# Kernel optimization log

Hardware: AMD Instinct MI355X
Metric: run time of the kernel (lower is better)

The kernel has to match this reference:

```python
import jax, jax.numpy as jnp
import numpy as np

B, T, C, H = 16, 2048, 1024, 64  # batch, seq (== block_size), n_embd, head_size


def setup_inputs() -> dict:
    key = jax.random.key(0)
    ks = jax.random.split(key, 4)
    s = 1.0 / np.sqrt(C)  # Linear default init scale
    return {
        "x": jax.random.normal(ks[0], (B, T, C), dtype=jnp.float32),
        "Wq": jax.random.normal(ks[1], (C, H), dtype=jnp.float32) * s,
        "bq": jnp.zeros((H,), dtype=jnp.float32),
        "Wk": jax.random.normal(ks[2], (C, H), dtype=jnp.float32) * s,
        "bk": jnp.zeros((H,), dtype=jnp.float32),
        "Wv": jax.random.normal(ks[3], (C, H), dtype=jnp.float32) * s,
        "bv": jnp.zeros((H,), dtype=jnp.float32),
    }


def reference(x, Wq, bq, Wk, bk, Wv, bv):
    # q, k, v: (B, T, H)
    q = x @ Wq + bq
    k = x @ Wk + bk
    v = x @ Wv + bv
    # scores (B, T, T); NOTE: original code has NO 1/sqrt(H) scaling
    wei = jnp.einsum("btd,bsd->bts", q, k)
    t = x.shape[1]
    causal = jnp.tril(jnp.ones((t, t), dtype=bool))
    wei = jnp.where(causal, wei, -jnp.inf)
    # NOTE: original code applies softmax over dim=1 (query axis), kept faithfully
    wei = jax.nn.softmax(wei, axis=1)
    # dropout is identity at p=0 / eval
    out = jnp.einsum("bts,bsd->btd", wei, v)  # (B, T, H)
    return out
```

## Files before the change

### kernel.cpp

```cpp
#include <hip/hip_runtime.h>
#include <hip/hip_bf16.h>
#include <math.h>

#define TT 2048
#define NB 16

typedef short short8 __attribute__((ext_vector_type(8)));
typedef float f32x4 __attribute__((ext_vector_type(4)));
typedef unsigned short us4 __attribute__((ext_vector_type(4)));

#define MFMA16(a,b,c) __builtin_amdgcn_mfma_f32_16x16x32_bf16((a),(b),(c),0,0,0)

typedef const __attribute__((address_space(1))) unsigned gas_u32;
typedef __attribute__((address_space(3))) unsigned las_u32;

__device__ __forceinline__ void gll16(const void* g, void* l) {
    __builtin_amdgcn_global_load_lds((gas_u32*)g, (las_u32*)l, 16, 0, 0);
}

__device__ __forceinline__ unsigned short bf16rn(float f) {
    unsigned u = __float_as_uint(f);
    u += 0x7FFFu + ((u >> 16) & 1u);
    return (unsigned short)(u >> 16);
}
__device__ __forceinline__ float bf16tof(unsigned short h) {
    return __uint_as_float(((unsigned)h) << 16);
}

__device__ __forceinline__ int strip_base(int i) {
    int h = i >> 1;
    return h * (h + 1) + (i & 1) * (h + 1);
}

__global__ void wprep_kernel(const float* __restrict__ Wq,
                             const float* __restrict__ Wk,
                             const float* __restrict__ Wv,
                             short* __restrict__ WT)
{
    const int m = blockIdx.x >> 6, n = blockIdx.x & 63, tid = threadIdx.x;
    const float* W = (m == 0) ? Wq : ((m == 1) ? Wk : Wv);
    const float sc = (m == 0) ? 1.4426950408889634f : 1.f;
    const int k0 = tid * 4;
    us4 hv, lv;
#pragma unroll
    for (int r = 0; r < 4; ++r) {
        float v = W[(size_t)(k0 + r) * 64 + n] * sc;
        unsigned short hh = bf16rn(v);
        hv[r] = hh;
        lv[r] = bf16rn(v - bf16tof(hh));
    }
    *(us4*)&WT[((size_t)(m * 2 + 0) * 64 + n) * 1024 + k0] = hv;
    *(us4*)&WT[((size_t)(m * 2 + 1) * 64 + n) * 1024 + k0] = lv;
}

__global__ void zero_kernel(float* __restrict__ p) {
    p[blockIdx.x * 256 + threadIdx.x] = 0.f;
}

__global__ __launch_bounds__(256, 2) void qkv_kernel(
    const float* __restrict__ x,
    const float* __restrict__ bq, const float* __restrict__ bk,
    const float* __restrict__ bv,
    const short* __restrict__ WT,
    short* __restrict__ qhl, short* __restrict__ khl, short* __restrict__ vT)
{
    __shared__ short xs[8192];
    __shared__ short ws[24576];
    const int tid = threadIdx.x;
    const int w = tid >> 6, l15 = tid & 15, g = (tid >> 4) & 3;
    const int t0 = blockIdx.x * 64;

    f32x4 acc[12];
    const f32x4 z = {0.f, 0.f, 0.f, 0.f};
#pragma unroll
    for (int i = 0; i < 12; ++i) acc[i] = z;

#pragma unroll 1
    for (int kc = 0; kc < 16; ++kc) {
#pragma unroll
        for (int p = 0; p < 12; ++p) {
            int u = tid + p * 256;
            int part = u / 1536; int r = u - part * 1536;
            int kk = r / 768;    int r2 = r - kk * 768;
            int n = r2 >> 2, g8 = r2 & 3;
            int m = n >> 6, nn = n & 63;
            const short* src = WT + (((size_t)((m * 2 + part) * 64 + nn)) << 10)
                                  + kc * 64 + kk * 32 + g8 * 8;
            gll16(src, &ws[((tid & ~63) + p * 256) * 8]);
        }
#pragma unroll
        for (int p = 0; p < 2; ++p) {
            int idx = tid + p * 256;
            int kk = idx >> 8; int rem = idx & 255;
            int row = rem >> 2, g8 = rem & 3;
            const float* xp = x + (size_t)(t0 + row) * 1024 + kc * 64 + kk * 32 + g8 * 8;
            f32x4 a = *(const f32x4*)xp;
            f32x4 b2 = *(const f32x4*)(xp + 4);
            short8 h8, l8;
#pragma unroll
            for (int j = 0; j < 4; ++j) {
                unsigned short hh = bf16rn(a[j]);
                h8[j] = (short)hh; l8[j] = (short)bf16rn(a[j] - bf16tof(hh));
                hh = bf16rn(b2[j]);
                h8[j + 4] = (short)hh; l8[j + 4] = (short)bf16rn(b2[j] - bf16tof(hh));
            }
            *(short8*)&xs[((kk * 64 + row) * 4 + g8) * 8] = h8;
            *(short8*)&xs[(((2 + kk) * 64 + row) * 4 + g8) * 8] = l8;
        }
        __syncthreads();

#pragma unroll
        for (int kk = 0; kk < 2; ++kk) {
            short8 xf[2];
#pragma unroll
            for (int part = 0; part < 2; ++part)
                xf[part] = *(const short8*)
                    &xs[(((part * 2 + kk) * 64 + w * 16 + l15) * 4 + g) * 8];
#pragma unroll
            for (int Nb = 0; Nb < 12; ++Nb) {
                short8 wh = *(const short8*)&ws[((kk * 192 + Nb * 16 + l15) * 4 + g) * 8];
                if (Nb < 8) {
                    short8 wl = *(const short8*)
                        &ws[(((2 + kk) * 192 + Nb * 16 + l15) * 4 + g) * 8];
                    acc[Nb] = MFMA16(wh, xf[0], acc[Nb]);
                    acc[Nb] = MFMA16(wh, xf[1], acc[Nb]);
                    acc[Nb] = MFMA16(wl, xf[0], acc[Nb]);
                } else {
                    acc[Nb] = MFMA16(xf[0], wh, acc[Nb]);
                }
            }
        }
        __syncthreads();
    }

    const float LOG2E = 1.4426950408889634f;
#pragma unroll
    for (int Nb = 0; Nb < 12; ++Nb) {
        f32x4 a = acc[Nb];
        if (Nb < 8) {
            const bool isq = (Nb < 4);
            const int nbase = (Nb & 3) * 16 + g * 4;
            const int trow = t0 + w * 16 + l15;
            const float* bias = isq ? bq : bk;
            us4 hv, lv;
#pragma unroll
            for (int r = 0; r < 4; ++r) {
                float v = a[r] + (isq ? bias[nbase + r] * LOG2E : bias[nbase + r]);
                unsigned short hh = bf16rn(v);
                hv[r] = hh; lv[r] = bf16rn(v - bf16tof(hh));
            }
            short* dst = (isq ? qhl : khl) + ((size_t)trow * 2) * 64 + nbase;
            *(us4*)dst = hv;
            *(us4*)(dst + 64) = lv;
        } else {
            const int d = (Nb - 8) * 16 + l15;
            const int tbase = t0 + w * 16 + g * 4;
            const float bvd = bv[d];
            us4 pk;
#pragma unroll
            for (int r = 0; r < 4; ++r) pk[r] = bf16rn(a[r] + bvd);
            const int b = tbase >> 11, ttl = tbase & 2047;
            *(us4*)&vT[((size_t)(b * 64 + d)) * 2048 + ttl] = pk;
        }
    }
}

__global__ __launch_bounds__(256, 4) void colstatsP_kernel(
    const short* __restrict__ qhl, const short* __restrict__ khl,
    float* __restrict__ dcol, short* __restrict__ Pst)
{
    __shared__ short kb[8192];
    __shared__ short qb[8192];
    const int tid = threadIdx.x;
    const int w = tid >> 6, l15 = tid & 15, g = (tid >> 4) & 3;
    const int sblk = blockIdx.x, tc = blockIdx.y, b = blockIdx.z;
    const int tt0 = max(sblk, tc * 8), tt1 = min(32, tc * 8 + 8);
    if (tt0 >= tt1) return;
    const int s0 = sblk * 64;
    const int sl = w * 16 + g * 4;
    const int kgs = w >> 1, g8s = (w & 1) * 2 + (g >> 1), j0 = (g & 1) * 4;

#pragma unroll
    for (int p = 0; p < 4; ++p) {
        int u = tid + p * 256;
        int part = u >> 9, kk = (u >> 8) & 1, row = (u >> 2) & 63, g8 = u & 3;
        gll16(khl + ((size_t)(b * TT + s0 + row) * 2 + part) * 64 + kk * 32 + g8 * 8,
              &kb[((tid & ~63) + p * 256) * 8]);
    }

    short8 kf[2][2];
    float dsl[4] = {0.f, 0.f, 0.f, 0.f};
    const f32x4 z = {0.f, 0.f, 0.f, 0.f};

#pragma unroll 1
    for (int tt = tt0; tt < tt1; ++tt) {
#pragma unroll
        for (int p = 0; p < 4; ++p) {
            int u = tid + p * 256;
            int part = u >> 9, kk = (u >> 8) & 1, row = (u >> 2) & 63, g8 = u & 3;
            gll16(qhl + ((size_t)(b * TT + tt * 64 + row) * 2 + part) * 64 + kk * 32 + g8 * 8,
                  &qb[((tid & ~63) + p * 256) * 8]);
        }
        __syncthreads();
        if (tt == tt0) {
#pragma unroll
            for (int kk = 0; kk < 2; ++kk)
#pragma unroll
                for (int part = 0; part < 2; ++part)
                    kf[kk][part] = *(const short8*)
                        &kb[(((part * 2 + kk) * 64 + w * 16 + l15) * 4 + g) * 8];
        }
#pragma unroll
        for (int tb = 0; tb < 4; ++tb) {
            f32x4 a = z;
#pragma unroll
            for (int kk = 0; kk < 2; ++kk) {
                short8 qh = *(const short8*)&qb[((kk * 64 + tb * 16 + l15) * 4 + g) * 8];
                short8 ql = *(const short8*)&qb[(((2 + kk) * 64 + tb * 16 + l15) * 4 + g) * 8];
                a = MFMA16(kf[kk][0], qh, a);
                a = MFMA16(kf[kk][0], ql, a);
                a = MFMA16(kf[kk][1], qh, a);
            }
            if (tt == sblk) {
#pragma unroll
                for (int r = 0; r < 4; ++r)
                    if (tb * 16 + l15 < sl + r) a[r] = -INFINITY;
            }
            us4 pk;
#pragma unroll
            for (int r = 0; r < 4; ++r) {
                float p = exp2f(a[r]);
                dsl[r] += p;
                pk[r] = bf16rn(p);
            }
            const int strip = tt * 2 + (tb >> 1);
            const int t32 = (tb & 1) * 16 + l15;
            size_t toff = ((size_t)(b * 1056 + strip_base(strip) + sblk)) * 2048
                        + ((kgs * 32 + t32) * 4 + g8s) * 8 + j0;
            *(us4*)&Pst[toff] = pk;
        }
        __syncthreads();
    }
#pragma unroll
    for (int r = 0; r < 4; ++r) {
        float dv = dsl[r];
        dv += __shfl_xor(dv, 1); dv += __shfl_xor(dv, 2);
        dv += __shfl_xor(dv, 4); dv += __shfl_xor(dv, 8);
        dsl[r] = dv;
    }
    if (l15 == 0) {
#pragma unroll
        for (int r = 0; r < 4; ++r)
            atomicAdd(&dcol[(size_t)b * TT + s0 + sl + r], dsl[r]);
    }
}

__global__ void vprep_kernel(const short* __restrict__ vT,
                             const float* __restrict__ dcol,
                             short* __restrict__ vT2)
{
    const int u = blockIdx.x * 256 + threadIdx.x;
    const int s8 = u & 255, bd = u >> 8;
    const int b = bd >> 6;
    short8 v = *(const short8*)&vT[(size_t)bd * 2048 + s8 * 8];
    f32x4 d0 = *(const f32x4*)&dcol[(size_t)b * TT + s8 * 8];
    f32x4 d1 = *(const f32x4*)&dcol[(size_t)b * TT + s8 * 8 + 4];
    short8 o;
#pragma unroll
    for (int j = 0; j < 4; ++j) {
        o[j]     = (short)bf16rn(bf16tof((unsigned short)v[j])     / d0[j]);
        o[4 + j] = (short)bf16rn(bf16tof((unsigned short)v[4 + j]) / d1[j]);
    }
    *(short8*)&vT2[(size_t)bd * 2048 + s8 * 8] = o;
}

__global__ __launch_bounds__(256, 4) void attnout_kernel(
    const short* __restrict__ Pst, const short* __restrict__ vT2,
    float* __restrict__ out)
{
    __shared__ short vb[2][4096];
    __shared__ short ebA[2][2048];
    __shared__ short ebB[2][2048];
    const int tid = threadIdx.x;
    const int w = tid >> 6, l15 = tid & 15, g = (tid >> 4) & 3;
    const int p = blockIdx.x, b = blockIdx.y;
    const int iA = p, iB = 63 - p;
    const int nA = iA >> 1, nB = iB >> 1;
    const int sl = w * 16 + g * 4;

    const short* PA = Pst + ((size_t)(b * 1056 + strip_base(iA))) * 2048;
    const short* PB = Pst + ((size_t)(b * 1056 + strip_base(iB))) * 2048;
    const short* vbase = vT2 + (size_t)b * 64 * 2048;
    const int ldsu = (tid & ~63) * 8;

    auto stage = [&](int ss, int buf) {
#pragma unroll
        for (int pp = 0; pp < 2; ++pp) {
            int u = tid + pp * 256;
            int kgs = u >> 8, d = (u >> 2) & 63, g8 = u & 3;
            gll16(vbase + ((size_t)d) * 2048 + ss * 64 + kgs * 32 + g8 * 8,
                  &vb[buf][ldsu + pp * 2048]);
        }
        gll16(PB + (size_t)ss * 2048 + tid * 8, &ebB[buf][ldsu]);
        gll16(PA + (size_t)ss * 2048 + tid * 8, &ebA[buf][ldsu]);
    };

    f32x4 oaccA[2], oaccB[2];
    const f32x4 z = {0.f, 0.f, 0.f, 0.f};
    oaccA[0] = z; oaccA[1] = z; oaccB[0] = z; oaccB[1] = z;

    stage(0, 0);
#pragma unroll 1
    for (int ss = 0; ss <= nB; ++ss) {
        const int nss = (ss < nB) ? ss + 1 : nB;
        stage(nss, (ss + 1) & 1);
        asm volatile("s_waitcnt vmcnt(4)" ::: "memory");
        __builtin_amdgcn_s_barrier();
        asm volatile("" ::: "memory");

        const int cb_ = ss & 1;
        short8 vf[2];
#pragma unroll
        for (int kg = 0; kg < 2; ++kg)
            vf[kg] = *(const short8*)&vb[cb_][((kg * 64 + w * 16 + l15) * 4 + g) * 8];
#pragma unroll
        for (int tb = 0; tb < 2; ++tb)
#pragma unroll
            for (int kg = 0; kg < 2; ++kg) {
                short8 ef = *(const short8*)&ebB[cb_][((kg * 32 + tb * 16 + l15) * 4 + g) * 8];
                oaccB[tb] = MFMA16(vf[kg], ef, oaccB[tb]);
            }
        if (ss <= nA) {
#pragma unroll
            for (int tb = 0; tb < 2; ++tb)
#pragma unroll
                for (int kg = 0; kg < 2; ++kg) {
                    short8 ef = *(const short8*)&ebA[cb_][((kg * 32 + tb * 16 + l15) * 4 + g) * 8];
                    oaccA[tb] = MFMA16(vf[kg], ef, oaccA[tb]);
                }
        }
        asm volatile("" ::: "memory");
        __builtin_amdgcn_s_barrier();
    }

#pragma unroll
    for (int tb = 0; tb < 2; ++tb) {
        const int tA = iA * 32 + tb * 16 + l15;
        const int tB = iB * 32 + tb * 16 + l15;
        *(f32x4*)(out + ((size_t)(b * TT + tA)) * 64 + sl) = oaccA[tb];
        *(f32x4*)(out + ((size_t)(b * TT + tB)) * 64 + sl) = oaccB[tb];
    }
}

extern "C" void kernel_launch(void* const* d_in, const int* in_sizes, int n_in,
                              void* d_out, int out_size, void* d_ws, size_t ws_size,
                              hipStream_t stream)
{
    const float* x  = (const float*)d_in[0];
    const float* Wq = (const float*)d_in[1];
    const float* bq = (const float*)d_in[2];
    const float* Wk = (const float*)d_in[3];
    const float* bk = (const float*)d_in[4];
    const float* Wv = (const float*)d_in[5];
    const float* bv = (const float*)d_in[6];

    char* wsb = (char*)d_ws;
    short* qhl  = (short*)wsb;
    short* khl  = (short*)(wsb + 8388608);
    short* vTb  = (short*)(wsb + 16777216);
    short* vT2  = (short*)(wsb + 20971520);
    short* WT   = (short*)(wsb + 25165824);
    float* dcol = (float*)(wsb + 25952256);
    short* Pst  = (short*)(wsb + 26083328);

    zero_kernel<<<dim3(128), 256, 0, stream>>>(dcol);
    wprep_kernel<<<dim3(192), 256, 0, stream>>>(Wq, Wk, Wv, WT);
    qkv_kernel<<<dim3(512), 256, 0, stream>>>(x, bq, bk, bv, WT, qhl, khl, vTb);
    colstatsP_kernel<<<dim3(32, 4, NB), 256, 0, stream>>>(qhl, khl, dcol, Pst);
    vprep_kernel<<<dim3(1024), 256, 0, stream>>>(vTb, dcol, vT2);
    attnout_kernel<<<dim3(32, NB), 256, 0, stream>>>(Pst, vT2, (float*)d_out);
}
```

Measured before the change: 295.7 us.

## Double-buffer async LDS staging in QKV projection and column-stats kernels

The QKV projection kernel now double-buffers both the weight tiles and the fp32 x tiles in LDS. The next K chunk is loaded with async global-to-LDS copies while the current one is consumed. x is loaded raw into a swizzled fp32 buffer, and the bf16 hi/lo split now happens at fragment-read time, removing the register round-trip through the old conversion stage. The column-stats kernel double-buffers Q tiles the same way and hoists the K fragment load out of the loop. Both kernels use explicit vmcnt waits with bare barriers. The extra LDS lowers the occupancy hints (2→1 and 4→3), which can reduce latency hiding across blocks.

```diff
diff --git a/kernel.cpp b/kernel.cpp
--- a/kernel.cpp
+++ b/kernel.cpp
@@ -57,26 +57,27 @@
     p[blockIdx.x * 256 + threadIdx.x] = 0.f;
 }
 
-__global__ __launch_bounds__(256, 2) void qkv_kernel(
+__global__ __launch_bounds__(256, 1) void qkv_kernel(
     const float* __restrict__ x,
     const float* __restrict__ bq, const float* __restrict__ bk,
     const float* __restrict__ bv,
     const short* __restrict__ WT,
     short* __restrict__ qhl, short* __restrict__ khl, short* __restrict__ vT)
 {
-    __shared__ short xs[8192];
-    __shared__ short ws[24576];
+    __shared__ short ws[2][24576];
+    __shared__ float xsf[2][2][64][32];
     const int tid = threadIdx.x;
     const int w = tid >> 6, l15 = tid & 15, g = (tid >> 4) & 3;
     const int t0 = blockIdx.x * 64;
+    const int u0x = (2 * g) ^ (l15 & 7);
+    const int u1x = (2 * g + 1) ^ (l15 & 7);
 
     f32x4 acc[12];
     const f32x4 z = {0.f, 0.f, 0.f, 0.f};
 #pragma unroll
     for (int i = 0; i < 12; ++i) acc[i] = z;
 
-#pragma unroll 1
-    for (int kc = 0; kc < 16; ++kc) {
+    auto stageW = [&](int kc, int buf) {
 #pragma unroll
         for (int p = 0; p < 12; ++p) {
             int u = tid + p * 256;
@@ -86,51 +87,62 @@
             int m = n >> 6, nn = n & 63;
             const short* src = WT + (((size_t)((m * 2 + part) * 64 + nn)) << 10)
                                   + kc * 64 + kk * 32 + g8 * 8;
-            gll16(src, &ws[((tid & ~63) + p * 256) * 8]);
-        }
-#pragma unroll
-        for (int p = 0; p < 2; ++p) {
-            int idx = tid + p * 256;
-            int kk = idx >> 8; int rem = idx & 255;
-            int row = rem >> 2, g8 = rem & 3;
-            const float* xp = x + (size_t)(t0 + row) * 1024 + kc * 64 + kk * 32 + g8 * 8;
-            f32x4 a = *(const f32x4*)xp;
-            f32x4 b2 = *(const f32x4*)(xp + 4);
-            short8 h8, l8;
+            gll16(src, &ws[buf][((tid & ~63) + p * 256) * 8]);
+        }
+    };
+    auto stageX = [&](int kc, int buf) {
+#pragma unroll
+        for (int p = 0; p < 4; ++p) {
+            int u = tid + p * 256;
+            int kk = u >> 9, rem = u & 511;
+            int row = rem >> 3, ul = rem & 7;
+            int uu = ul ^ (row & 7);
+            gll16(x + (size_t)(t0 + row) * 1024 + kc * 64 + kk * 32 + uu * 4,
+                  &xsf[buf][0][0][0] + ((tid & ~63) + p * 256) * 4);
+        }
+    };
+
+    stageX(0, 0);
+    stageW(0, 0);
+#pragma unroll 1
+    for (int kc = 0; kc < 16; ++kc) {
+        const int buf = kc & 1;
+        if (kc < 15) {
+            stageX(kc + 1, buf ^ 1);
+            stageW(kc + 1, buf ^ 1);
+            asm volatile("s_waitcnt vmcnt(16)" ::: "memory");
+        } else {
+            asm volatile("s_waitcnt vmcnt(0)" ::: "memory");
+        }
+        __builtin_amdgcn_s_barrier();
+
+#pragma unroll
+        for (int kk = 0; kk < 2; ++kk) {
+            f32x4 lo4 = *(const f32x4*)&xsf[buf][kk][w * 16 + l15][u0x * 4];
+            f32x4 hi4 = *(const f32x4*)&xsf[buf][kk][w * 16 + l15][u1x * 4];
+            short8 xh, xl;
 #pragma unroll
             for (int j = 0; j < 4; ++j) {
-                unsigned short hh = bf16rn(a[j]);
-                h8[j] = (short)hh; l8[j] = (short)bf16rn(a[j] - bf16tof(hh));
-                hh = bf16rn(b2[j]);
-                h8[j + 4] = (short)hh; l8[j + 4] = (short)bf16rn(b2[j] - bf16tof(hh));
-            }
-            *(short8*)&xs[((kk * 64 + row) * 4 + g8) * 8] = h8;
-            *(short8*)&xs[(((2 + kk) * 64 + row) * 4 + g8) * 8] = l8;
-        }
-        __syncthreads();
-
-#pragma unroll
-        for (int kk = 0; kk < 2; ++kk) {
-            short8 xf[2];
-#pragma unroll
-            for (int part = 0; part < 2; ++part)
-                xf[part] = *(const short8*)
-                    &xs[(((part * 2 + kk) * 64 + w * 16 + l15) * 4 + g) * 8];
+                unsigned short hh = bf16rn(lo4[j]);
+                xh[j] = (short)hh; xl[j] = (short)bf16rn(lo4[j] - bf16tof(hh));
+                hh = bf16rn(hi4[j]);
+                xh[j + 4] = (short)hh; xl[j + 4] = (short)bf16rn(hi4[j] - bf16tof(hh));
+            }
 #pragma unroll
             for (int Nb = 0; Nb < 12; ++Nb) {
-                short8 wh = *(const short8*)&ws[((kk * 192 + Nb * 16 + l15) * 4 + g) * 8];
+                short8 wh = *(const short8*)&ws[buf][((kk * 192 + Nb * 16 + l15) * 4 + g) * 8];
                 if (Nb < 8) {
                     short8 wl = *(const short8*)
-                        &ws[(((2 + kk) * 192 + Nb * 16 + l15) * 4 + g) * 8];
-                    acc[Nb] = MFMA16(wh, xf[0], acc[Nb]);
-                    acc[Nb] = MFMA16(wh, xf[1], acc[Nb]);
-                    acc[Nb] = MFMA16(wl, xf[0], acc[Nb]);
+                        &ws[buf][(((2 + kk) * 192 + Nb * 16 + l15) * 4 + g) * 8];
+                    acc[Nb] = MFMA16(wh, xh, acc[Nb]);
+                    acc[Nb] = MFMA16(wh, xl, acc[Nb]);
+                    acc[Nb] = MFMA16(wl, xh, acc[Nb]);
                 } else {
-                    acc[Nb] = MFMA16(xf[0], wh, acc[Nb]);
+                    acc[Nb] = MFMA16(xh, wh, acc[Nb]);
                 }
             }
         }
-        __syncthreads();
+        __builtin_amdgcn_s_barrier();
     }
 
     const float LOG2E = 1.4426950408889634f;
@@ -165,12 +177,12 @@
     }
 }
 
-__global__ __launch_bounds__(256, 4) void colstatsP_kernel(
+__global__ __launch_bounds__(256, 3) void colstatsP_kernel(
     const short* __restrict__ qhl, const short* __restrict__ khl,
     float* __restrict__ dcol, short* __restrict__ Pst)
 {
     __shared__ short kb[8192];
-    __shared__ short qb[8192];
+    __shared__ short qb[2][8192];
     const int tid = threadIdx.x;
     const int w = tid >> 6, l15 = tid & 15, g = (tid >> 4) & 3;
     const int sblk = blockIdx.x, tc = blockIdx.y, b = blockIdx.z;
@@ -180,6 +192,16 @@
     const int sl = w * 16 + g * 4;
     const int kgs = w >> 1, g8s = (w & 1) * 2 + (g >> 1), j0 = (g & 1) * 4;
 
+    auto stageQ = [&](int tt, int buf) {
+#pragma unroll
+        for (int p = 0; p < 4; ++p) {
+            int u = tid + p * 256;
+            int part = u >> 9, kk = (u >> 8) & 1, row = (u >> 2) & 63, g8 = u & 3;
+            gll16(qhl + ((size_t)(b * TT + tt * 64 + row) * 2 + part) * 64 + kk * 32 + g8 * 8,
+                  &qb[buf][((tid & ~63) + p * 256) * 8]);
+        }
+    };
+
 #pragma unroll
     for (int p = 0; p < 4; ++p) {
         int u = tid + p * 256;
@@ -187,36 +209,39 @@
         gll16(khl + ((size_t)(b * TT + s0 + row) * 2 + part) * 64 + kk * 32 + g8 * 8,
               &kb[((tid & ~63) + p * 256) * 8]);
     }
+    stageQ(tt0, 0);
+    asm volatile("s_waitcnt vmcnt(0)" ::: "memory");
+    __builtin_amdgcn_s_barrier();
 
     short8 kf[2][2];
+#pragma unroll
+    for (int kk = 0; kk < 2; ++kk)
+#pragma unroll
+        for (int part = 0; part < 2; ++part)
+            kf[kk][part] = *(const short8*)
+                &kb[(((part * 2 + kk) * 64 + w * 16 + l15) * 4 + g) * 8];
+
     float dsl[4] = {0.f, 0.f, 0.f, 0.f};
     const f32x4 z = {0.f, 0.f, 0.f, 0.f};
+    int buf = 0;
 
 #pragma unroll 1
     for (int tt = tt0; tt < tt1; ++tt) {
-#pragma unroll
-        for (int p = 0; p < 4; ++p) {
-            int u = tid + p * 256;
-            int part = u >> 9, kk = (u >> 8) & 1, row = (u >> 2) & 63, g8 = u & 3;
-            gll16(qhl + ((size_t)(b * TT + tt * 64 + row) * 2 + part) * 64 + kk * 32 + g8 * 8,
-                  &qb[((tid & ~63) + p * 256) * 8]);
-        }
-        __syncthreads();
-        if (tt == tt0) {
-#pragma unroll
-            for (int kk = 0; kk < 2; ++kk)
-#pragma unroll
-                for (int part = 0; part < 2; ++part)
-                    kf[kk][part] = *(const short8*)
-                        &kb[(((part * 2 + kk) * 64 + w * 16 + l15) * 4 + g) * 8];
-        }
+        if (tt + 1 < tt1) {
+            stageQ(tt + 1, buf ^ 1);
+            asm volatile("s_waitcnt vmcnt(8)" ::: "memory");
+        } else {
+            asm volatile("s_waitcnt vmcnt(4)" ::: "memory");
+        }
+        __builtin_amdgcn_s_barrier();
+
 #pragma unroll
         for (int tb = 0; tb < 4; ++tb) {
             f32x4 a = z;
 #pragma unroll
             for (int kk = 0; kk < 2; ++kk) {
-                short8 qh = *(const short8*)&qb[((kk * 64 + tb * 16 + l15) * 4 + g) * 8];
-                short8 ql = *(const short8*)&qb[(((2 + kk) * 64 + tb * 16 + l15) * 4 + g) * 8];
+                short8 qh = *(const short8*)&qb[buf][((kk * 64 + tb * 16 + l15) * 4 + g) * 8];
+                short8 ql = *(const short8*)&qb[buf][(((2 + kk) * 64 + tb * 16 + l15) * 4 + g) * 8];
                 a = MFMA16(kf[kk][0], qh, a);
                 a = MFMA16(kf[kk][0], ql, a);
                 a = MFMA16(kf[kk][1], qh, a);
@@ -239,7 +264,8 @@
                         + ((kgs * 32 + t32) * 4 + g8s) * 8 + j0;
             *(us4*)&Pst[toff] = pk;
         }
-        __syncthreads();
+        __builtin_amdgcn_s_barrier();
+        buf ^= 1;
     }
 #pragma unroll
     for (int r = 0; r < 4; ++r) {
```

After: 328.9 us. 11.2% more time.
